# Optimization experiments

Measured on AMD Instinct MI355X. Metric: run time of the kernel, lower is better.

Reference implementation:

```python
import jax, jax.numpy as jnp
import numpy as np

N_NETWORKS = 4
BETA = 2.0          # CustomHopfield beta = 2.0
UPDATE_STEPS = 4    # update_steps_max=4 fixed-point iterations


def setup_inputs() -> dict:
    key = jax.random.key(0)
    k0, k1, k2, k3 = jax.random.split(key, 4)
    B, IN_DIM, E = 256, 784, 128          # batch hardcoded by repeat(256,...)
    N_EMB = 32768                          # stored patterns per network
    return {
        "x": jax.random.normal(k0, (B, IN_DIM), jnp.float32),
        # embeddings: [n_networks * n_emb, E + 1]; last column is dropped (keys = emb[..., :-1])
        "embeddings": jax.random.normal(k1, (N_NETWORKS * N_EMB, E + 1), jnp.float32),
        "W_enc": jax.random.normal(k2, (IN_DIM, E), jnp.float32) / np.float32(np.sqrt(IN_DIM)),
        "b_enc": jnp.zeros((E,), jnp.float32),
        "W_lin": jax.random.normal(k3, (E * N_NETWORKS, 10), jnp.float32) / np.float32(np.sqrt(E * N_NETWORKS)),
        "b_lin": jnp.zeros((10,), jnp.float32),
    }


def reference(x, embeddings, W_enc, b_enc, W_lin, b_lin):
    B = x.shape[0]
    E = W_enc.shape[1]
    # keys per Hopfield network: [N, K, E] (identity projections: input_size=1, num_heads=1)
    keys = embeddings[:, :-1].reshape(N_NETWORKS, -1, E)
    z = x @ W_enc + b_enc                                   # encoder -> [B, E]
    q = jnp.broadcast_to(z[None], (N_NETWORKS, B, E))       # each network queries same z
    for _ in range(UPDATE_STEPS):
        # modern continuous Hopfield update: q <- softmax(beta * q K^T) K
        attn = jax.nn.softmax(BETA * jnp.einsum('nbe,nke->nbk', q, keys), axis=-1)
        q = jnp.einsum('nbk,nke->nbe', attn, keys)
    z_cat = jnp.transpose(q, (1, 0, 2)).reshape(B, N_NETWORKS * E)  # concat per-network retrievals
    return jax.nn.log_softmax(jax.nn.relu(z_cat) @ W_lin + b_lin, axis=-1)
```

## Files before the change

### kernel.cpp

```cpp
#include <hip/hip_runtime.h>
#include <hip/hip_bf16.h>
#include <cstdint>
#include <cstddef>


#define NNET 4
#define NQ   256
#define EDIM 128
#define NKEY 32768
#define ESTR 129
#define QT   64
#define NCHUNK 32
#define KPC  (NKEY/NCHUNK)
#define KQ   256
#define SCAN_WAVES 4
#define NTILE 32
#define BLOCKCAP 64
#define SURV_CAP 512
#define WCAP 1024
#define MITCAP 128
#define EMIT_MARGIN 10.0f
#define SEL_MARGIN  9.5f
#define REL_MARGIN  9.75f

typedef _Float16 half8 __attribute__((ext_vector_type(8)));
typedef float f32x4v __attribute__((ext_vector_type(4)));

__device__ __forceinline__ float dec16(unsigned v) {
  _Float16 h = __builtin_bit_cast(_Float16, (unsigned short)(v & 0xFFFFu));
  return (float)h;
}
__device__ __forceinline__ unsigned pack16(int key, float s) {
  unsigned short hb = __builtin_bit_cast(unsigned short, (_Float16)s);
  return ((unsigned)key << 16) | (unsigned)hb;
}
__device__ __forceinline__ unsigned enc_f32(float f) {
  unsigned u = __float_as_uint(f);
  return (u & 0x80000000u) ? ~u : (u | 0x80000000u);
}
__device__ __forceinline__ float dec_f32(unsigned e) {
  unsigned u = (e & 0x80000000u) ? (e & 0x7FFFFFFFu) : ~e;
  return __uint_as_float(u);
}

__global__ __launch_bounds__(128)
void enc_kernel(const float* __restrict__ x, const float* __restrict__ We,
                const float* __restrict__ be, float* __restrict__ q0,
                int* __restrict__ gw) {
  const int b = blockIdx.x, tid = threadIdx.x;
  __shared__ float xs[784];
  for (int i = tid; i < 784; i += 128) xs[i] = x[b * 784 + i];
  __syncthreads();
  float acc = be[tid];
  for (int i = 0; i < 784; ++i) acc += xs[i] * We[i * EDIM + tid];
#pragma unroll
  for (int n = 0; n < NNET; ++n) q0[((size_t)n * NQ + b) * EDIM + tid] = acc;
  if (b == 0 && tid < 4) gw[tid] = 0;
}

typedef _Float16 half4v __attribute__((ext_vector_type(4)));
__global__ __launch_bounds__(256)
void keyprep_kernel(const float* __restrict__ emb, _Float16* __restrict__ kh) {
  const size_t quads = (size_t)NNET * NKEY * EDIM / 4;
  for (size_t i4 = (size_t)blockIdx.x * 256 + threadIdx.x; i4 < quads;
       i4 += (size_t)gridDim.x * 256) {
    const size_t row = i4 >> 5;
    const int col = (int)(i4 & 31) * 4;
    const float* src = emb + row * ESTR + col;
    half4v h;
#pragma unroll
    for (int j = 0; j < 4; ++j) h[j] = (_Float16)src[j];
    *(half4v*)(kh + i4 * 4) = h;
  }
}

template <bool F16K>
__global__ __launch_bounds__(SCAN_WAVES * 64)
void scan_kernel(const float* __restrict__ qcur, const float* __restrict__ emb,
                 const _Float16* __restrict__ keysh,
                 int* __restrict__ cntb, float* __restrict__ cmaxb,
                 unsigned* __restrict__ cand,
                 int* __restrict__ gw, int* __restrict__ wit) {
  const int wg = blockIdx.x;
  const int xcd = wg & 7;
  const int qt = (wg >> 3) & 3;
  const int window = wg >> 5;
  const int c = window * 8 + xcd;
  const int net = c >> 5, chunk = c & 31;

  const int tid = threadIdx.x;
  const int lane = tid & 63;
  const int w = tid >> 6;
  const int g = lane >> 4, ln = lane & 15;

  __shared__ _Float16 kbuf[2][32 * EDIM];
  __shared__ unsigned lmax[QT];
  __shared__ int lcnt[QT];
  __shared__ unsigned lbuf[QT][BLOCKCAP];
  if (tid < QT) { lmax[tid] = enc_f32(-3.4e38f); lcnt[tid] = 0; }

  half8 aq[4];
  {
    const float* qb = qcur + ((size_t)net * NQ + qt * QT + w * 16) * EDIM;
#pragma unroll
    for (int f = 0; f < 4; ++f) {
      const float* p = qb + ln * EDIM + f * 32 + g * 8;
      half8 h;
#pragma unroll
      for (int j = 0; j < 8; ++j) h[j] = (_Float16)(2.0f * p[j]);
      aq[f] = h;
    }
  }

  const int key0 = chunk * KPC;
  const _Float16* ksrc = F16K ? (keysh + ((size_t)net * NKEY + key0) * EDIM) : nullptr;
  const float* esrc = emb + ((size_t)net * NKEY + key0) * ESTR;

  const int sid0 = tid, sid1 = tid + 256;
  auto swzoff = [&](int sid) {
    const int key = sid >> 4, seg = sid & 15;
    return key * 256 + ((seg * 16) ^ ((key & 7) << 4));
  };
  const int woff0 = swzoff(sid0), woff1 = swzoff(sid1);

  auto loadSeg = [&](int tile, int sid) -> half8 {
    if constexpr (F16K) {
      return *(const half8*)(ksrc + (size_t)tile * 32 * EDIM + sid * 8);
    } else {
      const int key = sid >> 4, seg = sid & 15;
      const float* p = esrc + (size_t)(tile * 32 + key) * ESTR + seg * 8;
      half8 h;
#pragma unroll
      for (int j = 0; j < 8; ++j) h[j] = (_Float16)p[j];
      return h;
    }
  };

  {
    half8 r0 = loadSeg(0, sid0), r1 = loadSeg(0, sid1);
    *(half8*)((char*)kbuf[0] + woff0) = r0;
    *(half8*)((char*)kbuf[0] + woff1) = r1;
  }
  __syncthreads();

  float rowmax[4];
#pragma unroll
  for (int r = 0; r < 4; ++r) rowmax[r] = -3.4e38f;
  const int q0l = w * 16 + 4 * g;
  const int rmask = (ln & 7) << 4;

  for (int t = 0; t < NTILE; ++t) {
    const int cur = t & 1;
    const bool more = (t + 1) < NTILE;
    half8 r0, r1;
    if (more) { r0 = loadSeg(t + 1, sid0); r1 = loadSeg(t + 1, sid1); }

    f32x4v acc[2];
    acc[0] = f32x4v{0.f, 0.f, 0.f, 0.f};
    acc[1] = f32x4v{0.f, 0.f, 0.f, 0.f};
#pragma unroll
    for (int st = 0; st < 2; ++st) {
      const char* kb = (const char*)kbuf[cur] + (st * 16 + ln) * 256;
#pragma unroll
      for (int f = 0; f < 4; ++f) {
        const half8 bk = *(const half8*)(kb + ((f * 64 + g * 16) ^ rmask));
        acc[st] = __builtin_amdgcn_mfma_f32_16x16x32_f16(aq[f], bk, acc[st], 0, 0, 0);
      }
    }
#pragma unroll
    for (int st = 0; st < 2; ++st)
#pragma unroll
      for (int r = 0; r < 4; ++r) rowmax[r] = fmaxf(rowmax[r], acc[st][r]);
#pragma unroll
    for (int d = 1; d < 16; d <<= 1)
#pragma unroll
      for (int r = 0; r < 4; ++r)
        rowmax[r] = fmaxf(rowmax[r], __shfl_xor(rowmax[r], d, 64));
#pragma unroll
    for (int st = 0; st < 2; ++st) {
      const int keyg = key0 + t * 32 + st * 16 + ln;
#pragma unroll
      for (int r = 0; r < 4; ++r)
        if (acc[st][r] >= rowmax[r] - EMIT_MARGIN) {
          const int q = q0l + r;
          const int slot = atomicAdd(&lcnt[q], 1);
          if (slot < BLOCKCAP) lbuf[q][slot] = pack16(keyg, acc[st][r]);
        }
    }
    if (more) {
      *(half8*)((char*)kbuf[cur ^ 1] + woff0) = r0;
      *(half8*)((char*)kbuf[cur ^ 1] + woff1) = r1;
    }
    __syncthreads();
  }

  if (ln == 0) {
#pragma unroll
    for (int r = 0; r < 4; ++r)
      atomicMax(&lmax[q0l + r], enc_f32(rowmax[r]));
  }
  __syncthreads();

  const size_t qbase = (size_t)net * NQ + qt * QT;
  for (int j = tid; j < QT * BLOCKCAP; j += SCAN_WAVES * 64) {
    const int q = j >> 6, i = j & (BLOCKCAP - 1);
    const int cq = lcnt[q];
    if (i < (cq < BLOCKCAP ? cq : BLOCKCAP))
      cand[((qbase + q) * NCHUNK + chunk) * BLOCKCAP + i] = lbuf[q][i];
  }
  if (tid < QT) {
    const size_t cell = (qbase + tid) * NCHUNK + chunk;
    cntb[cell] = lcnt[tid];
    cmaxb[cell] = dec_f32(lmax[tid]);
    if (lcnt[tid] > BLOCKCAP) {
      int i = atomicAdd(gw, 4);
#pragma unroll
      for (int qq = 0; qq < 4; ++qq)
        if (i + qq < WCAP) wit[i + qq] = ((int)cell << 2) | qq;
    }
  }
}

__global__ __launch_bounds__(256)
void dense_kernel(const float* __restrict__ qcur, const float* __restrict__ emb,
                  const int* __restrict__ gw, const int* __restrict__ wit,
                  float* __restrict__ pm, float* __restrict__ pl,
                  float* __restrict__ po) {
  const int tid = threadIdx.x, lane = tid & 63, w = tid >> 6;
  const int grp = lane >> 3;
  const int le = lane & 7;
  int nwork = *gw;
  if (nwork > WCAP) nwork = WCAP;

  __shared__ float qv[EDIM];
  __shared__ float sc[KQ];
  __shared__ int klist[KQ];
  __shared__ float osh[EDIM];
  __shared__ float red[8];
  __shared__ int nsig;

  for (int it = blockIdx.x; it < nwork; it += gridDim.x) {
    const int v = wit[it];
    const int slot = v >> 7;
    const int chunk = (v >> 2) & 31;
    const int qq = v & 3;
    const int net = slot >> 8;
    const int kbase = chunk * KPC + qq * KQ;

    if (tid < EDIM) qv[tid] = 2.0f * qcur[(size_t)slot * EDIM + tid];
    if (tid == 0) nsig = 0;
    __syncthreads();

    const float* base = emb + ((size_t)net * NKEY + kbase) * ESTR;
    for (int pp = 0; pp < 8; pp += 4) {
      float s[4] = {0.f, 0.f, 0.f, 0.f};
      const float* kr[4];
#pragma unroll
      for (int u = 0; u < 4; ++u)
        kr[u] = base + (size_t)(w * 64 + (pp + u) * 8 + grp) * ESTR + le;
#pragma unroll
      for (int i = 0; i < 16; ++i) {
        const float qe = qv[le + 8 * i];
#pragma unroll
        for (int u = 0; u < 4; ++u) s[u] += qe * kr[u][8 * i];
      }
#pragma unroll
      for (int d = 1; d < 8; d <<= 1)
#pragma unroll
        for (int u = 0; u < 4; ++u) s[u] += __shfl_xor(s[u], d, 64);
      if (le == 0) {
#pragma unroll
        for (int u = 0; u < 4; ++u) sc[w * 64 + (pp + u) * 8 + grp] = s[u];
      }
    }
    __syncthreads();

    float m = sc[tid];
#pragma unroll
    for (int d = 32; d; d >>= 1) m = fmaxf(m, __shfl_xor(m, d, 64));
    if (lane == 0) red[w] = m;
    __syncthreads();
    const float m_c = fmaxf(fmaxf(red[0], red[1]), fmaxf(red[2], red[3]));

    const float ev = expf(sc[tid] - m_c);
    sc[tid] = ev;
    float l = ev;
#pragma unroll
    for (int d = 32; d; d >>= 1) l += __shfl_xor(l, d, 64);
    if (lane == 0) red[4 + w] = l;
    if (ev > 1e-9f) {
      const int pos = atomicAdd(&nsig, 1);
      klist[pos] = tid;
    }
    __syncthreads();
    const float l_c = red[4] + red[5] + red[6] + red[7];
    const int msig = nsig;

    const int e = tid & 127, hf = tid >> 7;
    float acc = 0.f;
    for (int j = hf; j < msig; j += 2) {
      const int kk = klist[j];
      acc += sc[kk] * emb[((size_t)net * NKEY + kbase + kk) * ESTR + e];
    }
    if (hf) osh[e] = acc;
    __syncthreads();
    if (!hf) po[(size_t)it * EDIM + e] = acc + osh[e];
    if (tid == 0) { pm[it] = m_c; pl[it] = l_c; }
    __syncthreads();
  }
}

__global__ __launch_bounds__(256)
void refine_kernel(const float* __restrict__ qcur, const float* __restrict__ emb,
                   const int* __restrict__ cntb, const float* __restrict__ cmaxb,
                   const unsigned* __restrict__ cand, float* __restrict__ qnext,
                   const int* __restrict__ gw, const int* __restrict__ wit,
                   const float* __restrict__ pm, const float* __restrict__ pl,
                   const float* __restrict__ po) {
  const int q = blockIdx.x, net = blockIdx.y;
  const int tid = threadIdx.x, lane = tid & 63, w = tid >> 6;
  const int slot = net * NQ + q;
  __shared__ float qv[EDIM];
  __shared__ float osh[EDIM];
  __shared__ int ccnt[NCHUNK];
  __shared__ float cmax[NCHUNK];
  __shared__ int keys[SURV_CAP];
  __shared__ float exsc[SURV_CAP];
  __shared__ int mit[MITCAP];
  __shared__ int nmit;
  __shared__ int nsurv;
  __shared__ float gmax_s;
  __shared__ float red[8];

  int nwork = *gw;
  if (nwork > WCAP) nwork = WCAP;

  if (tid < EDIM) qv[tid] = 2.0f * qcur[(size_t)slot * EDIM + tid];
  if (tid < NCHUNK) {
    ccnt[tid] = cntb[(size_t)slot * NCHUNK + tid];
    cmax[tid] = cmaxb[(size_t)slot * NCHUNK + tid];
  }
  if (tid == 0) { nsurv = 0; nmit = 0; }
  __syncthreads();
  if (tid == 0) {
    float gv = -3.4e38f;
    for (int c = 0; c < NCHUNK; ++c) gv = fmaxf(gv, cmax[c]);
    gmax_s = gv;
  }
  for (int it = tid; it < nwork; it += 256) {
    if ((wit[it] >> 7) == slot) {
      const int i = atomicAdd(&nmit, 1);
      if (i < MITCAP) mit[i] = it;
    }
  }
  __syncthreads();
  const float G = gmax_s;
  const int nm = nmit < MITCAP ? nmit : MITCAP;

  for (int j = tid; j < NCHUNK * BLOCKCAP; j += 256) {
    const int c = j >> 6, i = j & (BLOCKCAP - 1);
    if (cmax[c] < G - REL_MARGIN) continue;
    const int cc = ccnt[c];
    if (cc > BLOCKCAP) continue;
    if (i < cc) {
      const unsigned pv = cand[((size_t)slot * NCHUNK + c) * BLOCKCAP + i];
      if (dec16(pv) >= G - SEL_MARGIN) {
        const int k = atomicAdd(&nsurv, 1);
        if (k < SURV_CAP) keys[k] = (int)(pv >> 16);
      }
    }
  }
  __syncthreads();
  int m = nsurv < SURV_CAP ? nsurv : SURV_CAP;

  for (int j = w; j < m; j += 4) {
    const float* kr = emb + ((size_t)net * NKEY + keys[j]) * ESTR;
    float p2 = qv[2 * lane] * kr[2 * lane] + qv[2 * lane + 1] * kr[2 * lane + 1];
#pragma unroll
    for (int d = 32; d; d >>= 1) p2 += __shfl_xor(p2, d, 64);
    if (lane == 0) exsc[j] = p2;
  }
  __syncthreads();
  if (w == 0) {
    float em = -3.4e38f;
    for (int j = lane; j < m; j += 64) em = fmaxf(em, exsc[j]);
#pragma unroll
    for (int d = 32; d; d >>= 1) em = fmaxf(em, __shfl_xor(em, d, 64));
    if (lane == 0) red[0] = em;
  }
  __syncthreads();
  const float em = red[0];
  for (int j = tid; j < m; j += 256) exsc[j] = expf(exsc[j] - em);
  __syncthreads();
  if (w == 0) {
    float l = 0.f;
    for (int j = lane; j < m; j += 64) l += exsc[j];
#pragma unroll
    for (int d = 32; d; d >>= 1) l += __shfl_xor(l, d, 64);
    if (lane == 0) red[1] = l;
  }
  __syncthreads();

  if (tid == 0) {
    float mstar = (m > 0) ? em : -3.4e38f;
    for (int j = 0; j < nm; ++j) mstar = fmaxf(mstar, pm[mit[j]]);
    float ltot = (m > 0) ? red[1] * expf(em - mstar) : 0.f;
    for (int j = 0; j < nm; ++j) ltot += pl[mit[j]] * expf(pm[mit[j]] - mstar);
    red[2] = mstar;
    red[3] = ltot;
  }
  __syncthreads();
  const float mstar = red[2];
  const float inv = 1.0f / red[3];

  const int e = tid & 127, hf = tid >> 7;
  float acc = 0.f;
  for (int j = hf; j < m; j += 2)
    acc += exsc[j] * emb[((size_t)net * NKEY + keys[j]) * ESTR + e];
  if (hf) osh[e] = acc;
  __syncthreads();
  if (!hf) {
    float o = (m > 0) ? (acc + osh[e]) * expf(em - mstar) : 0.f;
    for (int j = 0; j < nm; ++j)
      o += po[(size_t)mit[j] * EDIM + e] * expf(pm[mit[j]] - mstar);
    qnext[(size_t)slot * EDIM + e] = o * inv;
  }
}

__global__ __launch_bounds__(64)
void head_kernel(const float* __restrict__ qf, const float* __restrict__ Wl,
                 const float* __restrict__ bl, float* __restrict__ out) {
  const int b = blockIdx.x, lane = threadIdx.x;
  float acc[10];
#pragma unroll
  for (int c = 0; c < 10; ++c) acc[c] = 0.f;
  for (int t = lane; t < NNET * EDIM; t += 64) {
    float z = qf[((size_t)(t >> 7) * NQ + b) * EDIM + (t & 127)];
    z = fmaxf(z, 0.f);
    const float* wr = Wl + t * 10;
#pragma unroll
    for (int c = 0; c < 10; ++c) acc[c] += z * wr[c];
  }
#pragma unroll
  for (int d = 32; d; d >>= 1)
#pragma unroll
    for (int c = 0; c < 10; ++c) acc[c] += __shfl_xor(acc[c], d, 64);
  if (lane == 0) {
    float lg[10], mxv = -3.4e38f;
#pragma unroll
    for (int c = 0; c < 10; ++c) {
      lg[c] = acc[c] + bl[c];
      mxv = fmaxf(mxv, lg[c]);
    }
    float s = 0.f;
#pragma unroll
    for (int c = 0; c < 10; ++c) s += expf(lg[c] - mxv);
    float lse = mxv + logf(s);
#pragma unroll
    for (int c = 0; c < 10; ++c) out[b * 10 + c] = lg[c] - lse;
  }
}

extern "C" void kernel_launch(void* const* d_in, const int* in_sizes, int n_in,
                              void* d_out, int out_size, void* d_ws, size_t ws_size,
                              hipStream_t stream) {
  (void)in_sizes; (void)n_in; (void)out_size;
  const float* x   = (const float*)d_in[0];
  const float* emb = (const float*)d_in[1];
  const float* We  = (const float*)d_in[2];
  const float* be  = (const float*)d_in[3];
  const float* Wl  = (const float*)d_in[4];
  const float* bl  = (const float*)d_in[5];
  float* out = (float*)d_out;

  char* p = (char*)d_ws;
  float* q0 = (float*)p;    p += (size_t)NNET * NQ * EDIM * 4;
  float* q1 = (float*)p;    p += (size_t)NNET * NQ * EDIM * 4;
  int* cntb = (int*)p;      p += (size_t)NNET * NQ * NCHUNK * 4;
  float* cmaxb = (float*)p; p += (size_t)NNET * NQ * NCHUNK * 4;
  unsigned* cand = (unsigned*)p; p += (size_t)NNET * NQ * NCHUNK * BLOCKCAP * 4;
  int* gw = (int*)p;        p += 16;
  int* wit = (int*)p;       p += (size_t)4 * WCAP * 4;
  float* pm = (float*)p;    p += (size_t)WCAP * 4;
  float* pl = (float*)p;    p += (size_t)WCAP * 4;
  float* po = (float*)p;    p += (size_t)WCAP * EDIM * 4;
  _Float16* kh = (_Float16*)p;
  const bool f16k =
      ((size_t)(p - (char*)d_ws) + (size_t)NNET * NKEY * EDIM * 2) <= ws_size;

  enc_kernel<<<dim3(NQ), dim3(128), 0, stream>>>(x, We, be, q0, gw);
  if (f16k)
    keyprep_kernel<<<dim3(4096), dim3(256), 0, stream>>>(emb, kh);

  const int nblocks = NNET * NCHUNK * (NQ / QT);
  float* qa = q0;
  float* qb = q1;
  for (int step = 0; step < 4; ++step) {
    int* gws = gw + step;
    int* wits = wit + step * WCAP;
    if (f16k)
      scan_kernel<true><<<dim3(nblocks), dim3(SCAN_WAVES * 64), 0, stream>>>(
          qa, emb, kh, cntb, cmaxb, cand, gws, wits);
    else
      scan_kernel<false><<<dim3(nblocks), dim3(SCAN_WAVES * 64), 0, stream>>>(
          qa, emb, (const _Float16*)nullptr, cntb, cmaxb, cand, gws, wits);
    dense_kernel<<<dim3(256), dim3(256), 0, stream>>>(qa, emb, gws, wits, pm, pl, po);
    refine_kernel<<<dim3(NQ, NNET), dim3(256), 0, stream>>>(
        qa, emb, cntb, cmaxb, cand, qb, gws, wits, pm, pl, po);
    float* t = qa; qa = qb; qb = t;
  }
  head_kernel<<<dim3(NQ), dim3(64), 0, stream>>>(qa, Wl, bl, out);
}
```

Baseline: 246.8 us.

## Double query tile per scan block and aggregate candidate emission with ballots

The scan kernel now covers 128 queries per block, with each wave holding two 16-row query fragments, so each key tile staged in LDS feeds twice as many MFMAs and total key traffic is halved. The row-max cross-lane reduction now runs only on some phases instead of every tile, and candidate emission uses wave ballots so one lane does a single LDS atomic per 16-lane group. The cost is half as many blocks, higher register use under launch_bounds(256,1), and a row max that can lag between reductions, which may let more candidates through the emit threshold.

```diff
diff --git a/kernel.cpp b/kernel.cpp
--- a/kernel.cpp
+++ b/kernel.cpp
@@ -9,12 +9,12 @@
 #define EDIM 128
 #define NKEY 32768
 #define ESTR 129
-#define QT   64
+#define QT   128
 #define NCHUNK 32
 #define KPC  (NKEY/NCHUNK)
 #define KQ   256
-#define SCAN_WAVES 4
-#define NTILE 32
+#define PKEYS 32
+#define NPHASE (KPC/PKEYS)
 #define BLOCKCAP 64
 #define SURV_CAP 512
 #define WCAP 1024
@@ -75,7 +75,7 @@
 }
 
 template <bool F16K>
-__global__ __launch_bounds__(SCAN_WAVES * 64)
+__global__ __launch_bounds__(256, 1)
 void scan_kernel(const float* __restrict__ qcur, const float* __restrict__ emb,
                  const _Float16* __restrict__ keysh,
                  int* __restrict__ cntb, float* __restrict__ cmaxb,
@@ -83,8 +83,8 @@
                  int* __restrict__ gw, int* __restrict__ wit) {
   const int wg = blockIdx.x;
   const int xcd = wg & 7;
-  const int qt = (wg >> 3) & 3;
-  const int window = wg >> 5;
+  const int qt = (wg >> 3) & 1;
+  const int window = wg >> 4;
   const int c = window * 8 + xcd;
   const int net = c >> 5, chunk = c & 31;
 
@@ -93,23 +93,25 @@
   const int w = tid >> 6;
   const int g = lane >> 4, ln = lane & 15;
 
-  __shared__ _Float16 kbuf[2][32 * EDIM];
+  __shared__ _Float16 kbuf[2][PKEYS * EDIM];
   __shared__ unsigned lmax[QT];
   __shared__ int lcnt[QT];
   __shared__ unsigned lbuf[QT][BLOCKCAP];
   if (tid < QT) { lmax[tid] = enc_f32(-3.4e38f); lcnt[tid] = 0; }
 
-  half8 aq[4];
+  half8 aq[2][4];
   {
-    const float* qb = qcur + ((size_t)net * NQ + qt * QT + w * 16) * EDIM;
-#pragma unroll
-    for (int f = 0; f < 4; ++f) {
-      const float* p = qb + ln * EDIM + f * 32 + g * 8;
-      half8 h;
-#pragma unroll
-      for (int j = 0; j < 8; ++j) h[j] = (_Float16)(2.0f * p[j]);
-      aq[f] = h;
-    }
+    const float* qb = qcur + ((size_t)net * NQ + qt * QT + w * 32) * EDIM;
+#pragma unroll
+    for (int a = 0; a < 2; ++a)
+#pragma unroll
+      for (int f = 0; f < 4; ++f) {
+        const float* p = qb + (a * 16 + ln) * EDIM + f * 32 + g * 8;
+        half8 h;
+#pragma unroll
+        for (int j = 0; j < 8; ++j) h[j] = (_Float16)(2.0f * p[j]);
+        aq[a][f] = h;
+      }
   }
 
   const int key0 = chunk * KPC;
@@ -125,10 +127,10 @@
 
   auto loadSeg = [&](int tile, int sid) -> half8 {
     if constexpr (F16K) {
-      return *(const half8*)(ksrc + (size_t)tile * 32 * EDIM + sid * 8);
+      return *(const half8*)(ksrc + (size_t)tile * PKEYS * EDIM + sid * 8);
     } else {
       const int key = sid >> 4, seg = sid & 15;
-      const float* p = esrc + (size_t)(tile * 32 + key) * ESTR + seg * 8;
+      const float* p = esrc + (size_t)(tile * PKEYS + key) * ESTR + seg * 8;
       half8 h;
 #pragma unroll
       for (int j = 0; j < 8; ++j) h[j] = (_Float16)p[j];
@@ -143,50 +145,70 @@
   }
   __syncthreads();
 
-  float rowmax[4];
-#pragma unroll
-  for (int r = 0; r < 4; ++r) rowmax[r] = -3.4e38f;
-  const int q0l = w * 16 + 4 * g;
+  float rowmax[8];
+#pragma unroll
+  for (int i = 0; i < 8; ++i) rowmax[i] = -3.4e38f;
   const int rmask = (ln & 7) << 4;
 
-  for (int t = 0; t < NTILE; ++t) {
+  for (int t = 0; t < NPHASE; ++t) {
     const int cur = t & 1;
-    const bool more = (t + 1) < NTILE;
+    const bool more = (t + 1) < NPHASE;
     half8 r0, r1;
     if (more) { r0 = loadSeg(t + 1, sid0); r1 = loadSeg(t + 1, sid1); }
 
-    f32x4v acc[2];
-    acc[0] = f32x4v{0.f, 0.f, 0.f, 0.f};
-    acc[1] = f32x4v{0.f, 0.f, 0.f, 0.f};
+    f32x4v acc[2][2];
+    acc[0][0] = f32x4v{0.f, 0.f, 0.f, 0.f};
+    acc[0][1] = f32x4v{0.f, 0.f, 0.f, 0.f};
+    acc[1][0] = f32x4v{0.f, 0.f, 0.f, 0.f};
+    acc[1][1] = f32x4v{0.f, 0.f, 0.f, 0.f};
 #pragma unroll
     for (int st = 0; st < 2; ++st) {
       const char* kb = (const char*)kbuf[cur] + (st * 16 + ln) * 256;
 #pragma unroll
       for (int f = 0; f < 4; ++f) {
         const half8 bk = *(const half8*)(kb + ((f * 64 + g * 16) ^ rmask));
-        acc[st] = __builtin_amdgcn_mfma_f32_16x16x32_f16(aq[f], bk, acc[st], 0, 0, 0);
+        acc[0][st] = __builtin_amdgcn_mfma_f32_16x16x32_f16(aq[0][f], bk, acc[0][st], 0, 0, 0);
+        acc[1][st] = __builtin_amdgcn_mfma_f32_16x16x32_f16(aq[1][f], bk, acc[1][st], 0, 0, 0);
       }
     }
 #pragma unroll
-    for (int st = 0; st < 2; ++st)
-#pragma unroll
-      for (int r = 0; r < 4; ++r) rowmax[r] = fmaxf(rowmax[r], acc[st][r]);
-#pragma unroll
-    for (int d = 1; d < 16; d <<= 1)
-#pragma unroll
-      for (int r = 0; r < 4; ++r)
-        rowmax[r] = fmaxf(rowmax[r], __shfl_xor(rowmax[r], d, 64));
-#pragma unroll
-    for (int st = 0; st < 2; ++st) {
-      const int keyg = key0 + t * 32 + st * 16 + ln;
-#pragma unroll
-      for (int r = 0; r < 4; ++r)
-        if (acc[st][r] >= rowmax[r] - EMIT_MARGIN) {
-          const int q = q0l + r;
-          const int slot = atomicAdd(&lcnt[q], 1);
-          if (slot < BLOCKCAP) lbuf[q][slot] = pack16(keyg, acc[st][r]);
+    for (int a = 0; a < 2; ++a)
+#pragma unroll
+      for (int st = 0; st < 2; ++st)
+#pragma unroll
+        for (int r = 0; r < 4; ++r)
+          rowmax[a * 4 + r] = fmaxf(rowmax[a * 4 + r], acc[a][st][r]);
+    if (t < 2 || (t & 3) == 3) {
+#pragma unroll
+      for (int d = 1; d < 16; d <<= 1)
+#pragma unroll
+        for (int i = 0; i < 8; ++i)
+          rowmax[i] = fmaxf(rowmax[i], __shfl_xor(rowmax[i], d, 64));
+    }
+#pragma unroll
+    for (int a = 0; a < 2; ++a)
+#pragma unroll
+      for (int r = 0; r < 4; ++r) {
+        const int q = w * 32 + a * 16 + 4 * g + r;
+        const float th = rowmax[a * 4 + r] - EMIT_MARGIN;
+#pragma unroll
+        for (int st = 0; st < 2; ++st) {
+          const bool e = acc[a][st][r] >= th;
+          const unsigned long long mb = __ballot(e);
+          const unsigned gm = (unsigned)((mb >> (16 * g)) & 0xFFFFu);
+          if (gm) {
+            const int ldr = (int)__builtin_ctz(gm);
+            int base = 0;
+            if (e && ln == ldr) base = atomicAdd(&lcnt[q], __popc(gm));
+            base = __shfl(base, 16 * g + ldr, 64);
+            if (e) {
+              const int slot = base + __popc(gm & ((1u << ln) - 1u));
+              if (slot < BLOCKCAP)
+                lbuf[q][slot] = pack16(key0 + t * PKEYS + st * 16 + ln, acc[a][st][r]);
+            }
+          }
         }
-    }
+      }
     if (more) {
       *(half8*)((char*)kbuf[cur ^ 1] + woff0) = r0;
       *(half8*)((char*)kbuf[cur ^ 1] + woff1) = r1;
@@ -196,13 +218,15 @@
 
   if (ln == 0) {
 #pragma unroll
-    for (int r = 0; r < 4; ++r)
-      atomicMax(&lmax[q0l + r], enc_f32(rowmax[r]));
+    for (int a = 0; a < 2; ++a)
+#pragma unroll
+      for (int r = 0; r < 4; ++r)
+        atomicMax(&lmax[w * 32 + a * 16 + 4 * g + r], enc_f32(rowmax[a * 4 + r]));
   }
   __syncthreads();
 
   const size_t qbase = (size_t)net * NQ + qt * QT;
-  for (int j = tid; j < QT * BLOCKCAP; j += SCAN_WAVES * 64) {
+  for (int j = tid; j < QT * BLOCKCAP; j += 256) {
     const int q = j >> 6, i = j & (BLOCKCAP - 1);
     const int cq = lcnt[q];
     if (i < (cq < BLOCKCAP ? cq : BLOCKCAP))
@@ -499,10 +523,10 @@
     int* gws = gw + step;
     int* wits = wit + step * WCAP;
     if (f16k)
-      scan_kernel<true><<<dim3(nblocks), dim3(SCAN_WAVES * 64), 0, stream>>>(
+      scan_kernel<true><<<dim3(nblocks), dim3(256), 0, stream>>>(
           qa, emb, kh, cntb, cmaxb, cand, gws, wits);
     else
-      scan_kernel<false><<<dim3(nblocks), dim3(SCAN_WAVES * 64), 0, stream>>>(
+      scan_kernel<false><<<dim3(nblocks), dim3(256), 0, stream>>>(
           qa, emb, (const _Float16*)nullptr, cntb, cmaxb, cand, gws, wits);
     dense_kernel<<<dim3(256), dim3(256), 0, stream>>>(qa, emb, gws, wits, pm, pl, po);
     refine_kernel<<<dim3(NQ, NNET), dim3(256), 0, stream>>>(
```

After: 388.7 us. +57.5%, slower.

## Stage key tiles via direct global-to-LDS loads and aggregate candidate emission atomics

Applied to the files above, without the earlier changes.

The fp16 key-tile prefetch now uses global_load_lds to write straight into LDS. The swizzle moves to the source addresses, so loads no longer pass through registers and a later store. The cross-lane rowmax reduction runs only on the first two tiles and every fourth tile after that; other tiles use a stale per-lane max, which loosens the emit threshold. Candidate emission uses a ballot plus one atomicAdd per 16-lane group instead of one atomic per surviving element. Risks: more candidates may be emitted because of the stale threshold, and the async LDS writes must be complete before the barrier.

```diff
diff --git a/kernel.cpp b/kernel.cpp
--- a/kernel.cpp
+++ b/kernel.cpp
@@ -42,6 +42,11 @@
   unsigned u = (e & 0x80000000u) ? (e & 0x7FFFFFFFu) : ~e;
   return __uint_as_float(u);
 }
+__device__ __forceinline__ void gload_lds16(const void* g, void* l) {
+  __builtin_amdgcn_global_load_lds(
+      (const __attribute__((address_space(1))) void*)g,
+      (__attribute__((address_space(3))) void*)l, 16, 0, 0);
+}
 
 __global__ __launch_bounds__(128)
 void enc_kernel(const float* __restrict__ x, const float* __restrict__ We,
@@ -116,31 +121,34 @@
   const _Float16* ksrc = F16K ? (keysh + ((size_t)net * NKEY + key0) * EDIM) : nullptr;
   const float* esrc = emb + ((size_t)net * NKEY + key0) * ESTR;
 
-  const int sid0 = tid, sid1 = tid + 256;
-  auto swzoff = [&](int sid) {
-    const int key = sid >> 4, seg = sid & 15;
-    return key * 256 + ((seg * 16) ^ ((key & 7) << 4));
+  auto stage = [&](int tile, int buf) {
+    if constexpr (F16K) {
+      const _Float16* tb = ksrc + (size_t)tile * 32 * EDIM;
+#pragma unroll
+      for (int i = 0; i < 2; ++i) {
+        const int sid = i * 256 + w * 64 + lane;
+        const int key = sid >> 4, segp = sid & 15;
+        const int seg = segp ^ (key & 7);
+        const _Float16* gp = tb + key * EDIM + seg * 8;
+        char* lp = (char*)kbuf[buf] + i * 4096 + w * 1024;
+        gload_lds16(gp, lp);
+      }
+    } else {
+#pragma unroll
+      for (int i = 0; i < 2; ++i) {
+        const int sid = i * 256 + tid;
+        const int key = sid >> 4, segp = sid & 15;
+        const int seg = segp ^ (key & 7);
+        const float* p = esrc + (size_t)(tile * 32 + key) * ESTR + seg * 8;
+        half8 h;
+#pragma unroll
+        for (int j = 0; j < 8; ++j) h[j] = (_Float16)p[j];
+        *(half8*)((char*)kbuf[buf] + sid * 16) = h;
+      }
+    }
   };
-  const int woff0 = swzoff(sid0), woff1 = swzoff(sid1);
-
-  auto loadSeg = [&](int tile, int sid) -> half8 {
-    if constexpr (F16K) {
-      return *(const half8*)(ksrc + (size_t)tile * 32 * EDIM + sid * 8);
-    } else {
-      const int key = sid >> 4, seg = sid & 15;
-      const float* p = esrc + (size_t)(tile * 32 + key) * ESTR + seg * 8;
-      half8 h;
-#pragma unroll
-      for (int j = 0; j < 8; ++j) h[j] = (_Float16)p[j];
-      return h;
-    }
-  };
-
-  {
-    half8 r0 = loadSeg(0, sid0), r1 = loadSeg(0, sid1);
-    *(half8*)((char*)kbuf[0] + woff0) = r0;
-    *(half8*)((char*)kbuf[0] + woff1) = r1;
-  }
+
+  stage(0, 0);
   __syncthreads();
 
   float rowmax[4];
@@ -151,9 +159,7 @@
 
   for (int t = 0; t < NTILE; ++t) {
     const int cur = t & 1;
-    const bool more = (t + 1) < NTILE;
-    half8 r0, r1;
-    if (more) { r0 = loadSeg(t + 1, sid0); r1 = loadSeg(t + 1, sid1); }
+    if (t + 1 < NTILE) stage(t + 1, cur ^ 1);
 
     f32x4v acc[2];
     acc[0] = f32x4v{0.f, 0.f, 0.f, 0.f};
@@ -171,25 +177,34 @@
     for (int st = 0; st < 2; ++st)
 #pragma unroll
       for (int r = 0; r < 4; ++r) rowmax[r] = fmaxf(rowmax[r], acc[st][r]);
-#pragma unroll
-    for (int d = 1; d < 16; d <<= 1)
-#pragma unroll
-      for (int r = 0; r < 4; ++r)
-        rowmax[r] = fmaxf(rowmax[r], __shfl_xor(rowmax[r], d, 64));
-#pragma unroll
-    for (int st = 0; st < 2; ++st) {
-      const int keyg = key0 + t * 32 + st * 16 + ln;
-#pragma unroll
-      for (int r = 0; r < 4; ++r)
-        if (acc[st][r] >= rowmax[r] - EMIT_MARGIN) {
-          const int q = q0l + r;
-          const int slot = atomicAdd(&lcnt[q], 1);
-          if (slot < BLOCKCAP) lbuf[q][slot] = pack16(keyg, acc[st][r]);
+    if (t < 2 || (t & 3) == 3) {
+#pragma unroll
+      for (int d = 1; d < 16; d <<= 1)
+#pragma unroll
+        for (int r = 0; r < 4; ++r)
+          rowmax[r] = fmaxf(rowmax[r], __shfl_xor(rowmax[r], d, 64));
+    }
+#pragma unroll
+    for (int r = 0; r < 4; ++r) {
+      const int q = q0l + r;
+      const float th = rowmax[r] - EMIT_MARGIN;
+#pragma unroll
+      for (int st = 0; st < 2; ++st) {
+        const bool e = acc[st][r] >= th;
+        const unsigned long long mb = __ballot(e);
+        const unsigned gm = (unsigned)((mb >> (16 * g)) & 0xFFFFu);
+        if (gm) {
+          const int ldr = (int)__builtin_ctz(gm);
+          int base = 0;
+          if (e && ln == ldr) base = atomicAdd(&lcnt[q], __popc(gm));
+          base = __shfl(base, 16 * g + ldr, 64);
+          if (e) {
+            const int slot = base + __popc(gm & ((1u << ln) - 1u));
+            if (slot < BLOCKCAP)
+              lbuf[q][slot] = pack16(key0 + t * 32 + st * 16 + ln, acc[st][r]);
+          }
         }
-    }
-    if (more) {
-      *(half8*)((char*)kbuf[cur ^ 1] + woff0) = r0;
-      *(half8*)((char*)kbuf[cur ^ 1] + woff1) = r1;
+      }
     }
     __syncthreads();
   }
```

Result: slower. 298.2 us (+20.8%).
